# Performance work log

Measured on AMD Instinct MI355X. Metric: run time of the kernel, lower is better.

The kernel has to match this reference:

```python
import jax, jax.numpy as jnp
import numpy as np

B, S, E, H = 4, 2048, 1024, 16
D = E // H  # head_dim = 64

def setup_inputs() -> dict:
    key = jax.random.key(0)
    k1, k2, k3 = jax.random.split(key, 3)
    x = jax.random.normal(k1, (B, S, E), dtype=jnp.float32)
    # Linear weights stored as [in, out] so y = x @ W (torch Linear uses W^T; same math).
    w_att = jax.random.normal(k2, (E, 3 * E), dtype=jnp.float32) * (1.0 / np.sqrt(E))
    w_proj = jax.random.normal(k3, (E, E), dtype=jnp.float32) * (1.0 / np.sqrt(E))
    return {"x": x, "w_att": w_att, "w_proj": w_proj}

def reference(x, w_att, w_proj):
    b, s, e = x.shape
    qkv = x @ w_att                      # [b, s, 3e]
    q, k, v = jnp.split(qkv, 3, axis=-1)
    # [b, h, s, d]
    q = q.reshape(b, s, H, D).transpose(0, 2, 1, 3)
    k = k.reshape(b, s, H, D).transpose(0, 2, 1, 3)
    v = v.reshape(b, s, H, D).transpose(0, 2, 1, 3)
    scale = 1.0 / np.sqrt(D)
    att = jnp.einsum('bhqd,bhkd->bhqk', q, k) * scale  # [b, h, s, s]
    causal = jnp.tril(jnp.ones((s, s), dtype=bool))
    att = jnp.where(causal[None, None], att, jnp.finfo(att.dtype).min)
    att = jax.nn.softmax(att, axis=-1)
    y = jnp.einsum('bhqk,bhkd->bhqd', att, v)          # [b, h, s, d]
    y = y.transpose(0, 2, 1, 3).reshape(b, s, e)
    return y @ w_proj
```

## Files before the change

kernel.cpp:

```cpp
#include <hip/hip_runtime.h>
#include <hip/hip_bf16.h>

typedef __bf16 b16v8 __attribute__((ext_vector_type(8)));
typedef __bf16 b16v4 __attribute__((ext_vector_type(4)));
typedef float  f32x4 __attribute__((ext_vector_type(4)));

#define BB 4
#define SS 2048
#define EE 1024
#define HH 16
#define DD 64

#define QSCALE 0.18033688011112042f

__device__ __forceinline__ void async16(const __bf16* g, __bf16* l) {
  typedef __attribute__((address_space(1))) const unsigned int gu32;
  typedef __attribute__((address_space(3))) unsigned int lu32;
  __builtin_amdgcn_global_load_lds((gu32*)g, (lu32*)l, 16, 0, 0);
}

__device__ __forceinline__ f32x4 mfma16x16x16_bf16(b16v4 a, b16v4 b, f32x4 c) {
#if __has_builtin(__builtin_amdgcn_mfma_f32_16x16x16_bf16)
  return __builtin_amdgcn_mfma_f32_16x16x16_bf16(a, b, c, 0, 0, 0);
#else
  typedef short s16v4 __attribute__((ext_vector_type(4)));
  union U { b16v4 h; s16v4 s; };
  U ua, ub; ua.h = a; ub.h = b;
  return __builtin_amdgcn_mfma_f32_16x16x16bf16_1k(ua.s, ub.s, c, 0, 0, 0);
#endif
}

__global__ __launch_bounds__(256) void cast_x_kernel(const float* __restrict__ in,
                                                     __bf16* __restrict__ out, int n4) {
  int i = blockIdx.x * 256 + threadIdx.x;
  if (i >= n4) return;
  float4 f = ((const float4*)in)[i];
  b16v4 o = {(__bf16)f.x, (__bf16)f.y, (__bf16)f.z, (__bf16)f.w};
  ((b16v4*)out)[i] = o;
}

__global__ __launch_bounds__(256) void cast_transpose(const float* __restrict__ w,
                                                      __bf16* __restrict__ wt, int K, int N) {
  __shared__ float t[32][33];
  int n0 = blockIdx.x * 32, k0 = blockIdx.y * 32;
  int tx = threadIdx.x & 31, ty = threadIdx.x >> 5;
#pragma unroll
  for (int j = 0; j < 32; j += 8)
    t[ty + j][tx] = w[(size_t)(k0 + ty + j) * N + n0 + tx];
  __syncthreads();
#pragma unroll
  for (int j = 0; j < 32; j += 8)
    wt[(size_t)(n0 + ty + j) * K + k0 + tx] = (__bf16)t[tx][ty + j];
}

__global__ __launch_bounds__(256) void transpose_v(const __bf16* __restrict__ vb,
                                                   __bf16* __restrict__ vtb) {
  __shared__ __bf16 t[64 * 72];
  const int s0 = blockIdx.x * 64;
  const int bh = blockIdx.y;
  const int tid = threadIdx.x;
  const __bf16* src = vb + ((size_t)bh * SS + s0) * DD;
#pragma unroll
  for (int i = 0; i < 2; ++i) {
    int c = tid + i * 256;
    *(uint4*)(t + (c >> 3) * 72 + (c & 7) * 8) =
        *(const uint4*)(src + (size_t)(c >> 3) * DD + (c & 7) * 8);
  }
  __syncthreads();
  __bf16* dst = vtb + (size_t)bh * DD * SS + s0;
#pragma unroll
  for (int i = 0; i < 2; ++i) {
    int c = tid + i * 256;
    int d = c >> 3, s8 = c & 7;
    union { __bf16 e[8]; uint4 v; } u;
#pragma unroll
    for (int k = 0; k < 8; ++k) u.e[k] = t[(s8 * 8 + k) * 72 + d];
    *(uint4*)(dst + (size_t)d * SS + s8 * 8) = u.v;
  }
}

template <int EPI>
__global__ __launch_bounds__(256) void gemm_bt(const __bf16* __restrict__ A,
                                               const __bf16* __restrict__ Bt,
                                               void* C0, void* C1, void* C2,
                                               int M, int N, int K) {
  __shared__ __bf16 a_lds[128 * 32];
  __shared__ __bf16 b_lds[128 * 32];
  const int tid = threadIdx.x;
  const int lane = tid & 63;
  const int w = tid >> 6;
  const int wm = (w >> 1) * 64, wn = (w & 1) * 64;
  const int l16 = lane & 15, quad = lane >> 4;
  const __bf16* Ab = A + (size_t)blockIdx.y * 128 * K;
  const __bf16* Bb = Bt + (size_t)blockIdx.x * 128 * K;
  f32x4 acc[4][4];
#pragma unroll
  for (int i = 0; i < 4; ++i)
#pragma unroll
    for (int j = 0; j < 4; ++j) acc[i][j] = f32x4{0.f, 0.f, 0.f, 0.f};

  for (int k0 = 0; k0 < K; k0 += 32) {
    __syncthreads();
#pragma unroll
    for (int i = 0; i < 2; ++i) {
      int c = tid + i * 256;
      async16(Ab + (size_t)(c >> 2) * K + k0 + (c & 3) * 8, a_lds + c * 8);
    }
#pragma unroll
    for (int i = 0; i < 2; ++i) {
      int c = tid + i * 256;
      async16(Bb + (size_t)(c >> 2) * K + k0 + (c & 3) * 8, b_lds + c * 8);
    }
    __syncthreads();
    b16v8 af[4], bf[4];
#pragma unroll
    for (int t = 0; t < 4; ++t) {
      af[t] = *(const b16v8*)(a_lds + (wm + t * 16 + l16) * 32 + quad * 8);
      bf[t] = *(const b16v8*)(b_lds + (wn + t * 16 + l16) * 32 + quad * 8);
    }
#pragma unroll
    for (int mt = 0; mt < 4; ++mt)
#pragma unroll
      for (int nt = 0; nt < 4; ++nt)
        acc[mt][nt] = __builtin_amdgcn_mfma_f32_16x16x32_bf16(af[mt], bf[nt], acc[mt][nt], 0, 0, 0);
  }

  if (EPI == 0) {
    __bf16* qb = (__bf16*)C0;
    __bf16* kb = (__bf16*)C1;
    __bf16* vb = (__bf16*)C2;
#pragma unroll
    for (int mt = 0; mt < 4; ++mt)
#pragma unroll
      for (int nt = 0; nt < 4; ++nt)
#pragma unroll
        for (int r = 0; r < 4; ++r) {
          int row = blockIdx.y * 128 + wm + mt * 16 + quad * 4 + r;
          int col = blockIdx.x * 128 + wn + nt * 16 + l16;
          float v = acc[mt][nt][r];
          int b = row >> 11, s = row & 2047;
          int sec = col >> 10, cc = col & 1023;
          int h = cc >> 6, d = cc & 63;
          size_t idx = (((size_t)(b * HH + h) * SS + s) << 6) + d;
          if (sec == 0) qb[idx] = (__bf16)(v * QSCALE);
          else if (sec == 1) kb[idx] = (__bf16)v;
          else vb[idx] = (__bf16)v;
        }
  } else {
    float* out = (float*)C0;
#pragma unroll
    for (int mt = 0; mt < 4; ++mt)
#pragma unroll
      for (int nt = 0; nt < 4; ++nt)
#pragma unroll
        for (int r = 0; r < 4; ++r) {
          int row = blockIdx.y * 128 + wm + mt * 16 + quad * 4 + r;
          int col = blockIdx.x * 128 + wn + nt * 16 + l16;
          out[(size_t)row * N + col] = acc[mt][nt][r];
        }
  }
}

__global__ __launch_bounds__(256, 2) void attn_kernel(const __bf16* __restrict__ qb,
                                                      const __bf16* __restrict__ kb,
                                                      const __bf16* __restrict__ vtb,
                                                      __bf16* __restrict__ y) {
  __shared__ __bf16 kv_lds[2][16384];
  const int tid = threadIdx.x;
  const int lane = tid & 63;
  const int w = tid >> 6;
  const int l16 = lane & 15, quad = lane >> 4;
  const int p = blockIdx.x, bh = blockIdx.y;
  const int b = bh >> 4, h = bh & 15;
  const __bf16* kbase = kb + (size_t)bh * SS * DD;
  const __bf16* vtbase = vtb + (size_t)bh * DD * SS;

  auto stage = [&](int j, __bf16* buf) {
#pragma unroll
    for (int i = 0; i < 4; ++i) {
      int L = w * 256 + i * 64 + lane;
      int row = L >> 3, c = L & 7;
      async16(kbase + (size_t)(j * 128 + row) * DD + ((c ^ (row & 7)) * 8), buf + L * 8);
    }
#pragma unroll
    for (int i = 0; i < 4; ++i) {
      int L = w * 256 + i * 64 + lane;
      int d = L >> 4, c = L & 15;
      async16(vtbase + (size_t)d * SS + j * 128 + ((c ^ (d & 15)) * 8), buf + 8192 + L * 8);
    }
  };

#pragma unroll
  for (int t = 0; t < 2; ++t) {
    const int qt = (t == 0) ? (15 - p) : p;

    b16v8 qf[2][2];
#pragma unroll
    for (int qtile = 0; qtile < 2; ++qtile)
#pragma unroll
      for (int ks = 0; ks < 2; ++ks)
        qf[qtile][ks] = *(const b16v8*)(qb + ((size_t)bh * SS + qt * 128 + w * 32 + qtile * 16 + l16) * DD + ks * 32 + quad * 8);

    f32x4 o[4][2];
#pragma unroll
    for (int dt = 0; dt < 4; ++dt)
#pragma unroll
      for (int qtile = 0; qtile < 2; ++qtile) o[dt][qtile] = f32x4{0.f, 0.f, 0.f, 0.f};
    float mrow[2] = {-1e30f, -1e30f}, lrow[2] = {0.f, 0.f};

    __syncthreads();
    stage(0, kv_lds[0]);

    for (int j = 0; j <= qt; ++j) {
      __syncthreads();
      if (j < qt) stage(j + 1, kv_lds[(j + 1) & 1]);
      const __bf16* kbuf = kv_lds[j & 1];
      const __bf16* vbuf = kbuf + 8192;

      f32x4 s[2][8];
#pragma unroll
      for (int qtile = 0; qtile < 2; ++qtile)
#pragma unroll
        for (int kf = 0; kf < 8; ++kf) s[qtile][kf] = f32x4{0.f, 0.f, 0.f, 0.f};
#pragma unroll
      for (int kf = 0; kf < 8; ++kf) {
        int rb = kf * 16 + l16;
        b16v8 kf0 = *(const b16v8*)(kbuf + rb * DD + ((quad ^ (rb & 7)) * 8));
        b16v8 kf1 = *(const b16v8*)(kbuf + rb * DD + (((quad + 4) ^ (rb & 7)) * 8));
#pragma unroll
        for (int qtile = 0; qtile < 2; ++qtile) {
          s[qtile][kf] = __builtin_amdgcn_mfma_f32_16x16x32_bf16(kf0, qf[qtile][0], s[qtile][kf], 0, 0, 0);
          s[qtile][kf] = __builtin_amdgcn_mfma_f32_16x16x32_bf16(kf1, qf[qtile][1], s[qtile][kf], 0, 0, 0);
        }
      }
      if (j == qt) {
#pragma unroll
        for (int qtile = 0; qtile < 2; ++qtile) {
          int ql = w * 32 + qtile * 16 + l16;
#pragma unroll
          for (int kf = 0; kf < 8; ++kf)
#pragma unroll
            for (int r = 0; r < 4; ++r)
              if (kf * 16 + quad * 4 + r > ql) s[qtile][kf][r] = -1e30f;
        }
      }
#pragma unroll
      for (int qtile = 0; qtile < 2; ++qtile) {
        float mx = s[qtile][0][0];
#pragma unroll
        for (int kf = 0; kf < 8; ++kf)
#pragma unroll
          for (int r = 0; r < 4; ++r) mx = fmaxf(mx, s[qtile][kf][r]);
        mx = fmaxf(mx, __shfl_xor(mx, 16));
        mx = fmaxf(mx, __shfl_xor(mx, 32));
        float mn = fmaxf(mrow[qtile], mx);
        float alpha = __builtin_amdgcn_exp2f(mrow[qtile] - mn);
        mrow[qtile] = mn;
        float rs = 0.f;
#pragma unroll
        for (int kf = 0; kf < 8; ++kf)
#pragma unroll
          for (int r = 0; r < 4; ++r) {
            float pv = __builtin_amdgcn_exp2f(s[qtile][kf][r] - mn);
            s[qtile][kf][r] = pv;
            rs += pv;
          }
        rs += __shfl_xor(rs, 16);
        rs += __shfl_xor(rs, 32);
        lrow[qtile] = lrow[qtile] * alpha + rs;
#pragma unroll
        for (int dt = 0; dt < 4; ++dt)
#pragma unroll
          for (int r = 0; r < 4; ++r) o[dt][qtile][r] *= alpha;
      }
#pragma unroll
      for (int kf = 0; kf < 8; ++kf) {
        b16v4 pf[2];
#pragma unroll
        for (int qtile = 0; qtile < 2; ++qtile) {
          b16v4 pk = {(__bf16)s[qtile][kf][0], (__bf16)s[qtile][kf][1],
                      (__bf16)s[qtile][kf][2], (__bf16)s[qtile][kf][3]};
          pf[qtile] = pk;
        }
        int cg = kf * 2 + (quad >> 1);
#pragma unroll
        for (int dt = 0; dt < 4; ++dt) {
          int d = dt * 16 + l16;
          b16v4 vf = *(const b16v4*)(vbuf + d * 128 + ((cg ^ l16) * 8) + ((quad & 1) * 4));
#pragma unroll
          for (int qtile = 0; qtile < 2; ++qtile)
            o[dt][qtile] = mfma16x16x16_bf16(vf, pf[qtile], o[dt][qtile]);
        }
      }
    }

#pragma unroll
    for (int qtile = 0; qtile < 2; ++qtile) {
      float inv = 1.0f / lrow[qtile];
      int q = qt * 128 + w * 32 + qtile * 16 + l16;
#pragma unroll
      for (int dt = 0; dt < 4; ++dt) {
        b16v4 ov = {(__bf16)(o[dt][qtile][0] * inv), (__bf16)(o[dt][qtile][1] * inv),
                    (__bf16)(o[dt][qtile][2] * inv), (__bf16)(o[dt][qtile][3] * inv)};
        *(b16v4*)(y + ((size_t)b * SS + q) * EE + h * 64 + dt * 16 + quad * 4) = ov;
      }
    }
  }
}

extern "C" void kernel_launch(void* const* d_in, const int* in_sizes, int n_in,
                              void* d_out, int out_size, void* d_ws, size_t ws_size,
                              hipStream_t stream) {
  (void)in_sizes; (void)n_in; (void)out_size; (void)ws_size;
  const float* x = (const float*)d_in[0];
  const float* w_att = (const float*)d_in[1];
  const float* w_proj = (const float*)d_in[2];
  float* out = (float*)d_out;

  char* ws = (char*)d_ws;
  size_t off = 0;
  auto alloc = [&](size_t elems) { __bf16* p = (__bf16*)(ws + off); off += elems * 2; return p; };
  __bf16* xb = alloc(8388608);
  __bf16* qb = alloc(8388608);
  __bf16* kb = alloc(8388608);
  __bf16* vb = alloc(8388608);
  __bf16* vtb = alloc(8388608);
  __bf16* watt = alloc(3145728);
  __bf16* wproj = alloc(1048576);

  cast_x_kernel<<<8192, 256, 0, stream>>>(x, xb, 2097152);
  cast_transpose<<<dim3(96, 32), 256, 0, stream>>>(w_att, watt, 1024, 3072);
  cast_transpose<<<dim3(32, 32), 256, 0, stream>>>(w_proj, wproj, 1024, 1024);
  gemm_bt<0><<<dim3(24, 64), 256, 0, stream>>>(xb, watt, qb, kb, vb, 8192, 3072, 1024);
  transpose_v<<<dim3(32, 64), 256, 0, stream>>>(vb, vtb);
  attn_kernel<<<dim3(8, 64), 256, 0, stream>>>(qb, kb, vtb, xb);
  gemm_bt<1><<<dim3(8, 64), 256, 0, stream>>>(xb, wproj, out, nullptr, nullptr, 8192, 1024, 1024);
}
```

Before: 265.6 us.

## Fuse V transpose into QKV GEMM epilogue and double-buffer GEMM LDS with swizzle

Removes the separate transpose_v kernel by writing V directly in transposed [b,h,d,s] layout from the QKV GEMM epilogue, saving a launch and an extra round trip of V through memory. The GEMM also gets double-buffered LDS tiles so the next K-slice load overlaps the current MFMA work, plus an XOR swizzle on LDS chunks to reduce bank conflicts. The transposed V stores are narrower and less coalesced, and LDS use doubles, which may affect occupancy.

Measured after the change: 256.6 us. -3.4%, faster.

```diff
diff --git a/kernel.cpp b/kernel.cpp
--- a/kernel.cpp
+++ b/kernel.cpp
@@ -53,39 +53,13 @@
     wt[(size_t)(n0 + ty + j) * K + k0 + tx] = (__bf16)t[tx][ty + j];
 }
 
-__global__ __launch_bounds__(256) void transpose_v(const __bf16* __restrict__ vb,
-                                                   __bf16* __restrict__ vtb) {
-  __shared__ __bf16 t[64 * 72];
-  const int s0 = blockIdx.x * 64;
-  const int bh = blockIdx.y;
-  const int tid = threadIdx.x;
-  const __bf16* src = vb + ((size_t)bh * SS + s0) * DD;
-#pragma unroll
-  for (int i = 0; i < 2; ++i) {
-    int c = tid + i * 256;
-    *(uint4*)(t + (c >> 3) * 72 + (c & 7) * 8) =
-        *(const uint4*)(src + (size_t)(c >> 3) * DD + (c & 7) * 8);
-  }
-  __syncthreads();
-  __bf16* dst = vtb + (size_t)bh * DD * SS + s0;
-#pragma unroll
-  for (int i = 0; i < 2; ++i) {
-    int c = tid + i * 256;
-    int d = c >> 3, s8 = c & 7;
-    union { __bf16 e[8]; uint4 v; } u;
-#pragma unroll
-    for (int k = 0; k < 8; ++k) u.e[k] = t[(s8 * 8 + k) * 72 + d];
-    *(uint4*)(dst + (size_t)d * SS + s8 * 8) = u.v;
-  }
-}
-
 template <int EPI>
 __global__ __launch_bounds__(256) void gemm_bt(const __bf16* __restrict__ A,
                                                const __bf16* __restrict__ Bt,
                                                void* C0, void* C1, void* C2,
                                                int M, int N, int K) {
-  __shared__ __bf16 a_lds[128 * 32];
-  __shared__ __bf16 b_lds[128 * 32];
+  __shared__ __bf16 a_lds[2][128 * 32];
+  __shared__ __bf16 b_lds[2][128 * 32];
   const int tid = threadIdx.x;
   const int lane = tid & 63;
   const int w = tid >> 6;
@@ -93,59 +67,74 @@
   const int l16 = lane & 15, quad = lane >> 4;
   const __bf16* Ab = A + (size_t)blockIdx.y * 128 * K;
   const __bf16* Bb = Bt + (size_t)blockIdx.x * 128 * K;
-  f32x4 acc[4][4];
-#pragma unroll
-  for (int i = 0; i < 4; ++i)
-#pragma unroll
-    for (int j = 0; j < 4; ++j) acc[i][j] = f32x4{0.f, 0.f, 0.f, 0.f};
-
-  for (int k0 = 0; k0 < K; k0 += 32) {
-    __syncthreads();
+
+  auto stage = [&](int k0, int bufi) {
 #pragma unroll
     for (int i = 0; i < 2; ++i) {
       int c = tid + i * 256;
-      async16(Ab + (size_t)(c >> 2) * K + k0 + (c & 3) * 8, a_lds + c * 8);
+      int row = c >> 2, ch = c & 3;
+      async16(Ab + (size_t)row * K + k0 + ((ch ^ (row & 3)) * 8), a_lds[bufi] + c * 8);
     }
 #pragma unroll
     for (int i = 0; i < 2; ++i) {
       int c = tid + i * 256;
-      async16(Bb + (size_t)(c >> 2) * K + k0 + (c & 3) * 8, b_lds + c * 8);
-    }
+      int row = c >> 2, ch = c & 3;
+      async16(Bb + (size_t)row * K + k0 + ((ch ^ (row & 3)) * 8), b_lds[bufi] + c * 8);
+    }
+  };
+
+  f32x4 acc[4][4];
+#pragma unroll
+  for (int i = 0; i < 4; ++i)
+#pragma unroll
+    for (int j = 0; j < 4; ++j) acc[i][j] = f32x4{0.f, 0.f, 0.f, 0.f};
+
+  stage(0, 0);
+  const int KT = K >> 5;
+  const int sw = (quad ^ (l16 & 3)) * 8;
+  for (int kt = 0; kt < KT; ++kt) {
     __syncthreads();
-    b16v8 af[4], bf[4];
+    if (kt + 1 < KT) stage((kt + 1) << 5, (kt + 1) & 1);
+    const __bf16* ab = a_lds[kt & 1];
+    const __bf16* bb = b_lds[kt & 1];
+    b16v8 af[4], bf4[4];
 #pragma unroll
     for (int t = 0; t < 4; ++t) {
-      af[t] = *(const b16v8*)(a_lds + (wm + t * 16 + l16) * 32 + quad * 8);
-      bf[t] = *(const b16v8*)(b_lds + (wn + t * 16 + l16) * 32 + quad * 8);
+      af[t] = *(const b16v8*)(ab + (wm + t * 16 + l16) * 32 + sw);
+      bf4[t] = *(const b16v8*)(bb + (wn + t * 16 + l16) * 32 + sw);
     }
 #pragma unroll
     for (int mt = 0; mt < 4; ++mt)
 #pragma unroll
       for (int nt = 0; nt < 4; ++nt)
-        acc[mt][nt] = __builtin_amdgcn_mfma_f32_16x16x32_bf16(af[mt], bf[nt], acc[mt][nt], 0, 0, 0);
+        acc[mt][nt] = __builtin_amdgcn_mfma_f32_16x16x32_bf16(af[mt], bf4[nt], acc[mt][nt], 0, 0, 0);
   }
 
   if (EPI == 0) {
     __bf16* qb = (__bf16*)C0;
     __bf16* kb = (__bf16*)C1;
-    __bf16* vb = (__bf16*)C2;
+    __bf16* vtb = (__bf16*)C2;
 #pragma unroll
     for (int mt = 0; mt < 4; ++mt)
 #pragma unroll
-      for (int nt = 0; nt < 4; ++nt)
-#pragma unroll
-        for (int r = 0; r < 4; ++r) {
-          int row = blockIdx.y * 128 + wm + mt * 16 + quad * 4 + r;
-          int col = blockIdx.x * 128 + wn + nt * 16 + l16;
-          float v = acc[mt][nt][r];
-          int b = row >> 11, s = row & 2047;
-          int sec = col >> 10, cc = col & 1023;
-          int h = cc >> 6, d = cc & 63;
-          size_t idx = (((size_t)(b * HH + h) * SS + s) << 6) + d;
-          if (sec == 0) qb[idx] = (__bf16)(v * QSCALE);
-          else if (sec == 1) kb[idx] = (__bf16)v;
-          else vb[idx] = (__bf16)v;
-        }
+      for (int nt = 0; nt < 4; ++nt) {
+        int row = blockIdx.y * 128 + wm + mt * 16 + quad * 4;
+        int col = blockIdx.x * 128 + wn + nt * 16 + l16;
+        int b = row >> 11, s = row & 2047;
+        int sec = col >> 10, cc = col & 1023;
+        int h = cc >> 6, d = cc & 63;
+        if (sec == 2) {
+          b16v4 vv = {(__bf16)acc[mt][nt][0], (__bf16)acc[mt][nt][1],
+                      (__bf16)acc[mt][nt][2], (__bf16)acc[mt][nt][3]};
+          *(b16v4*)(vtb + ((size_t)(b * HH + h) * DD + d) * SS + s) = vv;
+        } else {
+          __bf16* dst = (sec == 0) ? qb : kb;
+          float sc = (sec == 0) ? QSCALE : 1.0f;
+#pragma unroll
+          for (int r = 0; r < 4; ++r)
+            dst[(((size_t)(b * HH + h) * SS + s + r) << 6) + d] = (__bf16)(acc[mt][nt][r] * sc);
+        }
+      }
   } else {
     float* out = (float*)C0;
 #pragma unroll
@@ -323,7 +312,6 @@
   __bf16* xb = alloc(8388608);
   __bf16* qb = alloc(8388608);
   __bf16* kb = alloc(8388608);
-  __bf16* vb = alloc(8388608);
   __bf16* vtb = alloc(8388608);
   __bf16* watt = alloc(3145728);
   __bf16* wproj = alloc(1048576);
@@ -331,8 +319,7 @@
   cast_x_kernel<<<8192, 256, 0, stream>>>(x, xb, 2097152);
   cast_transpose<<<dim3(96, 32), 256, 0, stream>>>(w_att, watt, 1024, 3072);
   cast_transpose<<<dim3(32, 32), 256, 0, stream>>>(w_proj, wproj, 1024, 1024);
-  gemm_bt<0><<<dim3(24, 64), 256, 0, stream>>>(xb, watt, qb, kb, vb, 8192, 3072, 1024);
-  transpose_v<<<dim3(32, 64), 256, 0, stream>>>(vb, vtb);
+  gemm_bt<0><<<dim3(24, 64), 256, 0, stream>>>(xb, watt, qb, kb, vtb, 8192, 3072, 1024);
   attn_kernel<<<dim3(8, 64), 256, 0, stream>>>(qb, kb, vtb, xb);
   gemm_bt<1><<<dim3(8, 64), 256, 0, stream>>>(xb, wproj, out, nullptr, nullptr, 8192, 1024, 1024);
 }
```
